# Optimization experiments

Hardware: AMD Instinct MI355X
Metric: run time of the kernel (lower is better)

## Reference

```python
import jax, jax.numpy as jnp
import numpy as np

NEG_SLOPE = 0.2


def gat_conv(x, src, dst, W, a_src, a_dst, b, concat):
    # x: [N, Fin]; W: [H*C, Fin]; a_src/a_dst: [H, C]; b: [H*C] or [C]
    N = x.shape[0]
    H, C = a_src.shape
    h = (x @ W.T).reshape(N, H, C)                      # per-head transform
    s_n = jnp.sum(h * a_src, axis=-1)                   # [N, H]
    d_n = jnp.sum(h * a_dst, axis=-1)                   # [N, H]
    e = jax.nn.leaky_relu(s_n[src] + d_n[dst], NEG_SLOPE)  # [E, H]
    # segment softmax over incoming edges of each destination node
    m = jax.ops.segment_max(e, dst, num_segments=N)
    m = jnp.where(jnp.isfinite(m), m, 0.0)
    ex = jnp.exp(e - m[dst])
    denom = jax.ops.segment_sum(ex, dst, num_segments=N)
    alpha = ex / (denom[dst] + 1e-16)                    # [E, H]
    msg = h[src] * alpha[:, :, None]                     # [E, H, C]
    out = jax.ops.segment_sum(msg, dst, num_segments=N)  # [N, H, C]
    out = out.reshape(N, H * C) if concat else out.mean(axis=1)
    return out + b


def setup_inputs() -> dict:
    key = jax.random.key(0)
    ks = jax.random.split(key, 16)
    N, E, F, C, H = 50000, 800000, 256, 128, 4
    sc = lambda fan_in: 1.0 / np.sqrt(fan_in)
    inp = {
        "x": jax.random.normal(ks[0], (N, F), dtype=jnp.float32),
        "edge_index": jax.random.randint(ks[1], (2, E), 0, N, dtype=jnp.int64),
        # layer 1: F -> H*C (concat)
        "W1": jax.random.normal(ks[2], (H * C, F), jnp.float32) * sc(F),
        "a_src1": jax.random.normal(ks[3], (H, C), jnp.float32) * sc(C),
        "a_dst1": jax.random.normal(ks[4], (H, C), jnp.float32) * sc(C),
        "b1": jnp.zeros((H * C,), jnp.float32),
        # layer 2: H*C -> H*C (concat)
        "W2": jax.random.normal(ks[5], (H * C, H * C), jnp.float32) * sc(H * C),
        "a_src2": jax.random.normal(ks[6], (H, C), jnp.float32) * sc(C),
        "a_dst2": jax.random.normal(ks[7], (H, C), jnp.float32) * sc(C),
        "b2": jnp.zeros((H * C,), jnp.float32),
        # layer 3: H*C -> C (heads=1, concat=False)
        "W3": jax.random.normal(ks[8], (C, H * C), jnp.float32) * sc(H * C),
        "a_src3": jax.random.normal(ks[9], (1, C), jnp.float32) * sc(C),
        "a_dst3": jax.random.normal(ks[10], (1, C), jnp.float32) * sc(C),
        "b3": jnp.zeros((C,), jnp.float32),
        # allocation head: C -> C//2 -> 1
        "Wh1": jax.random.normal(ks[11], (C // 2, C), jnp.float32) * sc(C),
        "bh1": jnp.zeros((C // 2,), jnp.float32),
        "Wh2": jax.random.normal(ks[12], (1, C // 2), jnp.float32) * sc(C // 2),
        "bh2": jnp.zeros((1,), jnp.float32),
    }
    return inp


def reference(x, edge_index, W1, a_src1, a_dst1, b1, W2, a_src2, a_dst2, b2,
              W3, a_src3, a_dst3, b3, Wh1, bh1, Wh2, bh2):
    N = x.shape[0]
    loops = jnp.arange(N, dtype=edge_index.dtype)
    src = jnp.concatenate([edge_index[0], loops])  # self-loops (PyG default)
    dst = jnp.concatenate([edge_index[1], loops])

    h = gat_conv(x, src, dst, W1, a_src1, a_dst1, b1, concat=True)
    h = jax.nn.elu(h)  # dropout is identity at inference
    h = gat_conv(h, src, dst, W2, a_src2, a_dst2, b2, concat=True)
    h = jax.nn.elu(h)
    embeddings = gat_conv(h, src, dst, W3, a_src3, a_dst3, b3, concat=False)

    z = jax.nn.relu(embeddings @ Wh1.T + bh1)
    allocation_scores = jax.nn.sigmoid(z @ Wh2.T + bh2)
    return embeddings, allocation_scores
```

## Files before the change

### kernel.cpp

```cpp
#include <hip/hip_runtime.h>
#include <math.h>

typedef _Float16 f16;
typedef f16 f16x2 __attribute__((ext_vector_type(2)));
typedef f16 f16x8 __attribute__((ext_vector_type(8)));
typedef float f32x4 __attribute__((ext_vector_type(4)));

template <int V> struct VecT;
template <> struct VecT<2> { using T = f16 __attribute__((ext_vector_type(2))); };
template <> struct VecT<8> { using T = f16 __attribute__((ext_vector_type(8))); };

__device__ __forceinline__ unsigned ordf(float f) {
  unsigned u = __float_as_uint(f);
  return (u >> 31) ? ~u : (u | 0x80000000u);
}
__device__ __forceinline__ float unordf(unsigned u) {
  return (u >> 31) ? __uint_as_float(u & 0x7fffffffu) : __uint_as_float(~u);
}


__global__ void k_count(const int* __restrict__ dstArr, int* __restrict__ cnt,
                        int E, int Et) {
  int i = blockIdx.x * blockDim.x + threadIdx.x;
  if (i >= Et) return;
  int d = (i < E) ? dstArr[i] : (i - E);
  atomicAdd(&cnt[d], 1);
}

__global__ __launch_bounds__(256) void k_scanA(const int* __restrict__ cnt,
                                               int* __restrict__ row_ptr,
                                               int* __restrict__ bsum, int n) {
  __shared__ int part[256];
  int t = threadIdx.x;
  int base = blockIdx.x * 1024 + t * 4;
  int4 v = make_int4(0, 0, 0, 0);
  if (base + 3 < n) v = *(const int4*)&cnt[base];
  else {
    if (base + 0 < n) v.x = cnt[base + 0];
    if (base + 1 < n) v.y = cnt[base + 1];
    if (base + 2 < n) v.z = cnt[base + 2];
    if (base + 3 < n) v.w = cnt[base + 3];
  }
  int s = v.x + v.y + v.z + v.w;
  part[t] = s;
  __syncthreads();
  for (int off = 1; off < 256; off <<= 1) {
    int x = (t >= off) ? part[t - off] : 0;
    __syncthreads();
    part[t] += x;
    __syncthreads();
  }
  int p0 = (t == 0) ? 0 : part[t - 1];
  int p1 = p0 + v.x, p2 = p1 + v.y, p3 = p2 + v.z;
  if (base + 0 < n) row_ptr[base + 0] = p0;
  if (base + 1 < n) row_ptr[base + 1] = p1;
  if (base + 2 < n) row_ptr[base + 2] = p2;
  if (base + 3 < n) row_ptr[base + 3] = p3;
  if (t == 255) bsum[blockIdx.x] = part[255];
}

__global__ __launch_bounds__(1024) void k_scanB(int* __restrict__ bsum, int nb) {
  __shared__ int part[1024];
  int t = threadIdx.x;
  int v = (t < nb) ? bsum[t] : 0;
  part[t] = v;
  __syncthreads();
  for (int off = 1; off < 1024; off <<= 1) {
    int x = (t >= off) ? part[t - off] : 0;
    __syncthreads();
    part[t] += x;
    __syncthreads();
  }
  if (t < nb) bsum[t] = (t == 0) ? 0 : part[t - 1];
  if (t == 1023) bsum[nb] = part[1023];
}

__global__ void k_scanC(int* __restrict__ row_ptr, int* __restrict__ cursor,
                        const int* __restrict__ bsum, int n, int nb) {
  int i = blockIdx.x * blockDim.x + threadIdx.x;
  if (i < n) {
    int v = row_ptr[i] + bsum[i >> 10];
    row_ptr[i] = v;
    cursor[i] = v;
  }
  if (i == n) row_ptr[n] = bsum[nb];
}

__global__ void k_fill(const int* __restrict__ dstArr, int* __restrict__ cursor,
                       int* __restrict__ perm, int E, int Et) {
  int i = blockIdx.x * blockDim.x + threadIdx.x;
  if (i >= Et) return;
  int d = (i < E) ? dstArr[i] : (i - E);
  int pos = atomicAdd(&cursor[d], 1);
  perm[pos] = i;
}

__global__ void k_f2h4(const float* s0, f16* d0, int n0,
                       const float* s1, f16* d1, int n1,
                       const float* s2, f16* d2, int n2,
                       const float* s3, f16* d3, int n3) {
  int i = blockIdx.x * blockDim.x + threadIdx.x;
  const float* s; f16* d;
  if (i < n0) { s = s0; d = d0; }
  else if ((i -= n0) < n1) { s = s1; d = d1; }
  else if ((i -= n1) < n2) { s = s2; d = d2; }
  else if ((i -= n2) < n3) { s = s3; d = d3; }
  else return;
  float4 v = ((const float4*)s)[i];
  union { f16 h[4]; double dd; } u;
  u.h[0] = (f16)v.x; u.h[1] = (f16)v.y; u.h[2] = (f16)v.z; u.h[3] = (f16)v.w;
  ((double*)d)[i] = u.dd;
}

__global__ __launch_bounds__(256) void k_hgemm_nt(
    const f16* __restrict__ A, const f16* __restrict__ B,
    f16* __restrict__ C, int M, int Nn, int K,
    const float* __restrict__ a_src, const float* __restrict__ a_dst,
    float* __restrict__ sArr, float* __restrict__ dArr,
    unsigned* __restrict__ gmaxU, int H) {
  __shared__ f16 As[128 * 32];
  __shared__ f16 Bs[128 * 32];
  int tid = threadIdx.x;
  int wave = tid >> 6, lane = tid & 63;
  int quad = lane >> 4, l16 = lane & 15;
  int m0 = blockIdx.y * 128, n0 = blockIdx.x * 128;
  int wm = (wave & 1) * 64, wn = (wave >> 1) * 64;

  int lr = lane >> 2;
  int lc = lane & 3;
  int chunk = lc ^ ((lr >> 1) & 3);
  int rb0 = wave * 16;
  int rb1 = 64 + wave * 16;
  int ga0 = m0 + rb0 + lr; if (ga0 >= M) ga0 = M - 1;
  int ga1 = m0 + rb1 + lr; if (ga1 >= M) ga1 = M - 1;
  const f16* gA0 = A + (size_t)ga0 * K + chunk * 8;
  const f16* gA1 = A + (size_t)ga1 * K + chunk * 8;
  const f16* gB0 = B + (size_t)(n0 + rb0 + lr) * K + chunk * 8;
  const f16* gB1 = B + (size_t)(n0 + rb1 + lr) * K + chunk * 8;
  f16* lA0 = &As[rb0 * 32];
  f16* lA1 = &As[rb1 * 32];
  f16* lB0 = &Bs[rb0 * 32];
  f16* lB1 = &Bs[rb1 * 32];

  int rsw = (quad ^ ((l16 >> 1) & 3)) * 8;
  const f16* Ard[4];
  const f16* Brd[4];
#pragma unroll
  for (int i = 0; i < 4; ++i) {
    Ard[i] = &As[(wm + i * 16 + l16) * 32 + rsw];
    Brd[i] = &Bs[(wn + i * 16 + l16) * 32 + rsw];
  }

  f32x4 acc[4][4];
#pragma unroll
  for (int i = 0; i < 4; ++i)
#pragma unroll
    for (int j = 0; j < 4; ++j) acc[i][j] = (f32x4)(0.f);

  for (int k0 = 0; k0 < K; k0 += 32) {
    __syncthreads();
    __builtin_amdgcn_global_load_lds(
        (const __attribute__((address_space(1))) void*)(gA0 + k0),
        (__attribute__((address_space(3))) void*)lA0, 16, 0, 0);
    __builtin_amdgcn_global_load_lds(
        (const __attribute__((address_space(1))) void*)(gA1 + k0),
        (__attribute__((address_space(3))) void*)lA1, 16, 0, 0);
    __builtin_amdgcn_global_load_lds(
        (const __attribute__((address_space(1))) void*)(gB0 + k0),
        (__attribute__((address_space(3))) void*)lB0, 16, 0, 0);
    __builtin_amdgcn_global_load_lds(
        (const __attribute__((address_space(1))) void*)(gB1 + k0),
        (__attribute__((address_space(3))) void*)lB1, 16, 0, 0);
    __syncthreads();
    f16x8 af[4], bf[4];
#pragma unroll
    for (int i = 0; i < 4; ++i) af[i] = *(const f16x8*)Ard[i];
#pragma unroll
    for (int j = 0; j < 4; ++j) bf[j] = *(const f16x8*)Brd[j];
#pragma unroll
    for (int i = 0; i < 4; ++i)
#pragma unroll
      for (int j = 0; j < 4; ++j)
        acc[i][j] = __builtin_amdgcn_mfma_f32_16x16x32_f16(af[i], bf[j], acc[i][j], 0, 0, 0);
  }

#pragma unroll
  for (int i = 0; i < 4; ++i) {
#pragma unroll
    for (int r = 0; r < 4; ++r) {
      int m = m0 + wm + i * 16 + quad * 4 + r;
      if (m < M) {
        f16* Cp = C + (size_t)m * Nn + n0 + wn + l16;
#pragma unroll
        for (int j = 0; j < 4; ++j) Cp[j * 16] = (f16)acc[i][j][r];
      }
    }
  }

  float av[4], ad[4];
#pragma unroll
  for (int j = 0; j < 4; ++j) {
    int col = n0 + wn + l16 + j * 16;
    av[j] = a_src[col];
    ad[j] = a_dst[col];
  }
  float sp[16], dp[16];
#pragma unroll
  for (int i = 0; i < 4; ++i)
#pragma unroll
    for (int r = 0; r < 4; ++r) {
      float ss = 0.f, dd = 0.f;
#pragma unroll
      for (int j = 0; j < 4; ++j) {
        ss += acc[i][j][r] * av[j];
        dd += acc[i][j][r] * ad[j];
      }
#pragma unroll
      for (int msk = 1; msk < 16; msk <<= 1) {
        ss += __shfl_xor(ss, msk);
        dd += __shfl_xor(dd, msk);
      }
      sp[i * 4 + r] = ss;
      dp[i * 4 + r] = dd;
    }

  __syncthreads();
  float* fb = (float*)As;
  int wv = wn >> 6;
  if (l16 == 0) {
#pragma unroll
    for (int i = 0; i < 4; ++i)
#pragma unroll
      for (int r = 0; r < 4; ++r) {
        int row = wm + i * 16 + quad * 4 + r;
        fb[wv * 128 + row] = sp[i * 4 + r];
        fb[256 + wv * 128 + row] = dp[i * 4 + r];
      }
  }
  __syncthreads();
  if (tid < 128) {
    int m = m0 + tid;
    if (m < M) {
      float s = fb[tid] + fb[128 + tid];
      float d = fb[256 + tid] + fb[384 + tid];
      int head = n0 >> 7;
      sArr[(size_t)m * H + head] = s;
      dArr[(size_t)m * H + head] = d;
      atomicMax(&gmaxU[head], ordf(s));
    }
  }
}

template <int HH, int CT, bool DOELU, typename OutT>
__global__ __launch_bounds__(256) void k_aggregate(
    const f16* __restrict__ hin, const float* __restrict__ sArr,
    const float* __restrict__ dArr, const int* __restrict__ row_ptr,
    const int* __restrict__ perm, const int* __restrict__ srcArr,
    const unsigned* __restrict__ gmaxU, const float* __restrict__ bias,
    OutT* __restrict__ outp, int N, int E) {
  constexpr int VEC = CT / 64;
  constexpr int CPER = CT / HH;
  using gvec = typename VecT<VEC>::T;

  int n = blockIdx.x * 4 + (threadIdx.x >> 6);
  int lane = threadIdx.x & 63;
  if (n >= N) return;
  int e0 = row_ptr[n];
  int deg = row_ptr[n + 1] - e0;

  float dloc[HH], mn[HH];
#pragma unroll
  for (int h = 0; h < HH; ++h) {
    dloc[h] = dArr[n * HH + h];
    float m = unordf(gmaxU[h]) + dloc[h];
    mn[h] = (m > 0.f) ? m : 0.2f * m;
  }

  const int lanehead = (HH == 1) ? 0 : (lane * VEC) / CPER;
  float acc[VEC];
#pragma unroll
  for (int k = 0; k < VEC; ++k) acc[k] = 0.f;
  float denom[HH];
#pragma unroll
  for (int h = 0; h < HH; ++h) denom[h] = 0.f;

  for (int base = 0; base < deg; base += 64) {
    int cn = min(64, deg - base);
    int s_l = n;
    float w_l[HH];
#pragma unroll
    for (int h = 0; h < HH; ++h) w_l[h] = 0.f;
    if (lane < cn) {
      int eid = perm[e0 + base + lane];
      s_l = (eid < E) ? srcArr[eid] : (eid - E);
      if (HH == 4) {
        float4 sv = ((const float4*)sArr)[s_l];
        float svv[4] = {sv.x, sv.y, sv.z, sv.w};
#pragma unroll
        for (int h = 0; h < 4; ++h) {
          float e = svv[h] + dloc[h];
          e = (e > 0.f) ? e : 0.2f * e;
          w_l[h] = __expf(e - mn[h]);
        }
      } else {
        float e = sArr[s_l] + dloc[0];
        e = (e > 0.f) ? e : 0.2f * e;
        w_l[0] = __expf(e - mn[0]);
      }
    }
    for (int i = 0; i < cn; ++i) {
      int s = __shfl(s_l, i);
      float wh[HH];
#pragma unroll
      for (int h = 0; h < HH; ++h) {
        wh[h] = __shfl(w_l[h], i);
        denom[h] += wh[h];
      }
      float w = wh[lanehead];
      gvec v = *(const gvec*)(hin + (size_t)s * CT + lane * VEC);
#pragma unroll
      for (int k = 0; k < VEC; ++k) acc[k] += w * (float)v[k];
    }
  }

  float dn = denom[lanehead] + 1e-16f;
  struct alignas(sizeof(OutT) * VEC) OutV { OutT v[VEC]; } ov;
#pragma unroll
  for (int k = 0; k < VEC; ++k) {
    float v = acc[k] / dn + bias[lane * VEC + k];
    if (DOELU) v = (v > 0.f) ? v : expm1f(v);
    ov.v[k] = (OutT)v;
  }
  *(OutV*)(outp + (size_t)n * CT + lane * VEC) = ov;
}

__global__ __launch_bounds__(256) void k_head(
    const float* __restrict__ emb, const float* __restrict__ Wh1,
    const float* __restrict__ bh1, const float* __restrict__ Wh2,
    const float* __restrict__ bh2, float* __restrict__ scores, int N) {
  __shared__ float w1s[64 * 132];
  __shared__ float w2s[64];
  __shared__ float b1s[64];
  int t = threadIdx.x;
  for (int i = t; i < 64 * 32; i += 256) {
    int r = i >> 5, c4 = i & 31;
    float4 v = ((const float4*)Wh1)[i];
    *(float4*)&w1s[r * 132 + c4 * 4] = v;
  }
  if (t < 64) { w2s[t] = Wh2[t]; b1s[t] = bh1[t]; }
  __syncthreads();
  float b2v = bh2[0];
  int wave = t >> 6, lane = t & 63;
  int gw = blockIdx.x * 4 + wave;
  int nw = gridDim.x * 4;
  for (int n = gw; n < N; n += nw) {
    float2 xv = ((const float2*)(emb + (size_t)n * 128))[lane];
    float z = b1s[lane];
#pragma unroll
    for (int j = 0; j < 32; ++j) {
      float4 w = *(const float4*)&w1s[lane * 132 + 4 * j];
      float a0 = __shfl(xv.x, 2 * j);
      float a1 = __shfl(xv.y, 2 * j);
      float a2 = __shfl(xv.x, 2 * j + 1);
      float a3 = __shfl(xv.y, 2 * j + 1);
      z += w.x * a0 + w.y * a1 + w.z * a2 + w.w * a3;
    }
    z = fmaxf(z, 0.f);
    float v = z * w2s[lane];
#pragma unroll
    for (int off = 32; off; off >>= 1) v += __shfl_down(v, off);
    if (lane == 0) scores[n] = 1.f / (1.f + __expf(-(v + b2v)));
  }
}


extern "C" void kernel_launch(void* const* d_in, const int* in_sizes, int n_in,
                              void* d_out, int out_size, void* d_ws, size_t ws_size,
                              hipStream_t stream) {
  const float* x   = (const float*)d_in[0];
  const int*   ei  = (const int*)d_in[1];
  const float* W1  = (const float*)d_in[2];
  const float* as1 = (const float*)d_in[3];
  const float* ad1 = (const float*)d_in[4];
  const float* b1  = (const float*)d_in[5];
  const float* W2  = (const float*)d_in[6];
  const float* as2 = (const float*)d_in[7];
  const float* ad2 = (const float*)d_in[8];
  const float* b2  = (const float*)d_in[9];
  const float* W3  = (const float*)d_in[10];
  const float* as3 = (const float*)d_in[11];
  const float* ad3 = (const float*)d_in[12];
  const float* b3  = (const float*)d_in[13];
  const float* Wh1 = (const float*)d_in[14];
  const float* bh1 = (const float*)d_in[15];
  const float* Wh2 = (const float*)d_in[16];
  const float* bh2 = (const float*)d_in[17];
  float* out = (float*)d_out;

  const int F = 256, HC = 512, H = 4, C = 128;
  const int N = in_sizes[0] / F;
  const int E = in_sizes[1] / 2;
  const int Et = E + N;
  const int* srcArr = ei;
  const int* dstArr = ei + E;

  char* ws = (char*)d_ws;
  size_t off = 0;
  auto alloc = [&](size_t bytes) -> void* {
    void* p = ws + off;
    off += (bytes + 255) & ~(size_t)255;
    return p;
  };
  f16*   h16    = (f16*)alloc((size_t)N * HC * 2);
  f16*   hAgg   = (f16*)alloc((size_t)N * HC * 2);
  f16*   xh     = (f16*)alloc((size_t)N * F * 2);
  f16*   W1h    = (f16*)alloc((size_t)HC * F * 2);
  f16*   W2h    = (f16*)alloc((size_t)HC * HC * 2);
  f16*   W3h    = (f16*)alloc((size_t)C * HC * 2);
  int* row_ptr  = (int*)alloc((size_t)(N + 1) * 4);
  char* zr      = (char*)alloc((size_t)N * 4 + 64);
  int* cnt      = (int*)zr;
  unsigned* gm1 = (unsigned*)(zr + (size_t)N * 4);
  unsigned* gm2 = gm1 + 4;
  unsigned* gm3 = gm1 + 8;
  int* cursor   = (int*)alloc((size_t)N * 4);
  int* perm     = (int*)alloc((size_t)Et * 4);
  float* sArr   = (float*)alloc((size_t)N * H * 4);
  float* dArr   = (float*)alloc((size_t)N * H * 4);
  int* bsum     = (int*)alloc((size_t)1028 * 4);
  (void)ws_size; (void)n_in; (void)out_size;

  hipMemsetAsync(zr, 0, (size_t)N * 4 + 64, stream);
  int eb = (Et + 255) / 256;
  int nb = (N + 1023) / 1024;
  k_count<<<eb, 256, 0, stream>>>(dstArr, cnt, E, Et);
  k_scanA<<<nb, 256, 0, stream>>>(cnt, row_ptr, bsum, N);
  k_scanB<<<1, 1024, 0, stream>>>(bsum, nb);
  k_scanC<<<(N + 256) / 256, 256, 0, stream>>>(row_ptr, cursor, bsum, N, nb);
  k_fill<<<eb, 256, 0, stream>>>(dstArr, cursor, perm, E, Et);

  int c0 = N * F / 4, c1 = HC * F / 4, c2 = HC * HC / 4, c3 = C * HC / 4;
  int ctot = c0 + c1 + c2 + c3;
  k_f2h4<<<(ctot + 255) / 256, 256, 0, stream>>>(x, xh, c0, W1, W1h, c1,
                                                 W2, W2h, c2, W3, W3h, c3);

  int aggGrid = (N + 3) / 4;
  dim3 g1(HC / 128, (N + 127) / 128);
  dim3 g3(C / 128, (N + 127) / 128);

  k_hgemm_nt<<<g1, 256, 0, stream>>>(xh, W1h, h16, N, HC, F,
                                     as1, ad1, sArr, dArr, gm1, H);
  k_aggregate<4, 512, true, f16><<<aggGrid, 256, 0, stream>>>(
      h16, sArr, dArr, row_ptr, perm, srcArr, gm1, b1, hAgg, N, E);

  k_hgemm_nt<<<g1, 256, 0, stream>>>(hAgg, W2h, h16, N, HC, HC,
                                     as2, ad2, sArr, dArr, gm2, H);
  k_aggregate<4, 512, true, f16><<<aggGrid, 256, 0, stream>>>(
      h16, sArr, dArr, row_ptr, perm, srcArr, gm2, b2, hAgg, N, E);

  k_hgemm_nt<<<g3, 256, 0, stream>>>(hAgg, W3h, h16, N, C, HC,
                                     as3, ad3, sArr, dArr, gm3, 1);
  k_aggregate<1, 128, false, float><<<aggGrid, 256, 0, stream>>>(
      h16, sArr, dArr, row_ptr, perm, srcArr, gm3, b3, out, N, E);

  k_head<<<512, 256, 0, stream>>>(out, Wh1, bh1, Wh2, bh2, out + (size_t)N * C, N);
}
```

Before: 846.4 us.

## Stage edge offsets and weights in LDS and double-buffer gathers in aggregation

The aggregation kernel no longer broadcasts each edge's source index and weights through per-edge shuffles. Each wave now writes (byte offset, weight) pairs to shared memory and reads them back in groups of four, alternating between two register buffers so the next group's gathers are issued before the current group's FMAs. Denominators are summed per lane and reduced once with xor-shuffles at the end, so the shuffles are not repeated for every edge. This adds LDS traffic, a manual lgkmcnt wait and more registers, and it uses 32-bit byte offsets into the feature array.

```diff
diff --git a/kernel.cpp b/kernel.cpp
--- a/kernel.cpp
+++ b/kernel.cpp
@@ -262,11 +262,17 @@
   constexpr int CPER = CT / HH;
   using gvec = typename VecT<VEC>::T;
 
-  int n = blockIdx.x * 4 + (threadIdx.x >> 6);
+  __shared__ int2 pairs[4][64 * HH];
+
+  int wave = threadIdx.x >> 6;
   int lane = threadIdx.x & 63;
+  int n = blockIdx.x * 4 + wave;
   if (n >= N) return;
   int e0 = row_ptr[n];
   int deg = row_ptr[n + 1] - e0;
+
+  const int myhead = (HH == 1) ? 0 : (lane * VEC) / CPER;
+  const int laneByte = lane * VEC * 2;
 
   float dloc[HH], mn[HH];
 #pragma unroll
@@ -276,25 +282,44 @@
     mn[h] = (m > 0.f) ? m : 0.2f * m;
   }
 
-  const int lanehead = (HH == 1) ? 0 : (lane * VEC) / CPER;
   float acc[VEC];
 #pragma unroll
   for (int k = 0; k < VEC; ++k) acc[k] = 0.f;
-  float denom[HH];
-#pragma unroll
-  for (int h = 0; h < HH; ++h) denom[h] = 0.f;
+  float dsum[HH];
+#pragma unroll
+  for (int h = 0; h < HH; ++h) dsum[h] = 0.f;
+
+  int2* pw = &pairs[wave][0];
+
+#define LOADG(VB, WB, g)                                                      \
+  do {                                                                        \
+    _Pragma("unroll") for (int j_ = 0; j_ < 4; ++j_) {                        \
+      int2 p_ = pw[((g) * 4 + j_) * HH + myhead];                             \
+      WB[j_] = __int_as_float(p_.y);                                          \
+      VB[j_] = *(const gvec*)((const char*)hin + (unsigned)(p_.x + laneByte));\
+    }                                                                         \
+  } while (0)
+
+#define FMAG(VB, WB)                                                          \
+  do {                                                                        \
+    _Pragma("unroll") for (int j_ = 0; j_ < 4; ++j_)                          \
+        _Pragma("unroll") for (int k_ = 0; k_ < VEC; ++k_)                    \
+            acc[k_] += WB[j_] * (float)VB[j_][k_];                            \
+  } while (0)
 
   for (int base = 0; base < deg; base += 64) {
     int cn = min(64, deg - base);
-    int s_l = n;
+
+    int soff = 0;
     float w_l[HH];
 #pragma unroll
     for (int h = 0; h < HH; ++h) w_l[h] = 0.f;
     if (lane < cn) {
       int eid = perm[e0 + base + lane];
-      s_l = (eid < E) ? srcArr[eid] : (eid - E);
+      int s = (eid < E) ? srcArr[eid] : (eid - E);
+      soff = s * (CT * 2);
       if (HH == 4) {
-        float4 sv = ((const float4*)sArr)[s_l];
+        float4 sv = ((const float4*)sArr)[s];
         float svv[4] = {sv.x, sv.y, sv.z, sv.w};
 #pragma unroll
         for (int h = 0; h < 4; ++h) {
@@ -303,27 +328,66 @@
           w_l[h] = __expf(e - mn[h]);
         }
       } else {
-        float e = sArr[s_l] + dloc[0];
+        float e = sArr[s] + dloc[0];
         e = (e > 0.f) ? e : 0.2f * e;
         w_l[0] = __expf(e - mn[0]);
       }
     }
-    for (int i = 0; i < cn; ++i) {
-      int s = __shfl(s_l, i);
-      float wh[HH];
-#pragma unroll
-      for (int h = 0; h < HH; ++h) {
-        wh[h] = __shfl(w_l[h], i);
-        denom[h] += wh[h];
-      }
-      float w = wh[lanehead];
-      gvec v = *(const gvec*)(hin + (size_t)s * CT + lane * VEC);
-#pragma unroll
-      for (int k = 0; k < VEC; ++k) acc[k] += w * (float)v[k];
-    }
-  }
-
-  float dn = denom[lanehead] + 1e-16f;
+#pragma unroll
+    for (int h = 0; h < HH; ++h) dsum[h] += w_l[h];
+
+    if (HH == 4) {
+      int4 p0 = make_int4(soff, __float_as_int(w_l[0]), soff, __float_as_int(w_l[1]));
+      int4 p1 = make_int4(soff, __float_as_int(w_l[2]), soff, __float_as_int(w_l[3]));
+      *(int4*)&pw[lane * 4] = p0;
+      *(int4*)&pw[lane * 4 + 2] = p1;
+    } else {
+      pw[lane] = make_int2(soff, __float_as_int(w_l[0]));
+    }
+    asm volatile("s_waitcnt lgkmcnt(0)" ::: "memory");
+
+    int cng = (cn + 3) >> 2;
+    gvec vA[4], vB[4];
+    float wA[4], wB[4];
+    LOADG(vA, wA, 0);
+    int g = 0;
+    while (g + 2 < cng) {
+      LOADG(vB, wB, g + 1);
+      FMAG(vA, wA);
+      LOADG(vA, wA, g + 2);
+      FMAG(vB, wB);
+      g += 2;
+    }
+    if (g + 1 < cng) {
+      LOADG(vB, wB, g + 1);
+      FMAG(vA, wA);
+      FMAG(vB, wB);
+    } else {
+      FMAG(vA, wA);
+    }
+  }
+#undef LOADG
+#undef FMAG
+
+  float dn;
+  if (HH == 4) {
+    float t0 = dsum[0], t1 = dsum[1], t2 = dsum[2], t3 = dsum[3];
+#pragma unroll
+    for (int m = 1; m < 64; m <<= 1) {
+      t0 += __shfl_xor(t0, m);
+      t1 += __shfl_xor(t1, m);
+      t2 += __shfl_xor(t2, m);
+      t3 += __shfl_xor(t3, m);
+    }
+    dn = (myhead < 2) ? (myhead == 0 ? t0 : t1) : (myhead == 2 ? t2 : t3);
+  } else {
+    float t0 = dsum[0];
+#pragma unroll
+    for (int m = 1; m < 64; m <<= 1) t0 += __shfl_xor(t0, m);
+    dn = t0;
+  }
+  dn += 1e-16f;
+
   struct alignas(sizeof(OutT) * VEC) OutV { OutT v[VEC]; } ov;
 #pragma unroll
   for (int k = 0; k < VEC; ++k) {
```

New measurement: 846.4 us. Within noise of the previous version (-0.0%).
